# Performance work log

Hardware: AMD Instinct MI355X
Metric: run time of the kernel (lower is better)

## Reference

```python
import jax, jax.numpy as jnp
import numpy as np

# static config (matches init_kwargs)
NH, NKV, E, K = 16, 4, 8, 2
CAP_FACTOR = 1.25
LN_EPS = 1e-5


def _layer_norm(x, w, b):
    mu = jnp.mean(x, axis=-1, keepdims=True)
    var = jnp.mean(jnp.square(x - mu), axis=-1, keepdims=True)
    return (x - mu) * jax.lax.rsqrt(var + LN_EPS) * w + b


def setup_inputs() -> dict:
    key = jax.random.key(0)
    ks = jax.random.split(key, 6)
    S, B, H, F = 2048, 1, 1024, 2048
    HD = H // NH
    qkv_out = NKV * ((NH // NKV) + 2) * HD  # 1536
    f32 = jnp.float32
    return {
        "hidden_states": jax.random.normal(ks[0], (S, B, H), f32),
        "ln1_weight": jnp.ones((H,), f32),
        "ln1_bias": jnp.zeros((H,), f32),
        "ln2_weight": jnp.ones((H,), f32),
        "ln2_bias": jnp.zeros((H,), f32),
        "qkv_weight": jax.random.normal(ks[1], (qkv_out, H), f32) * 0.02,
        "proj_weight": jax.random.normal(ks[2], (H, H), f32) * 0.02,
        "router_weight": jax.random.normal(ks[3], (H, E), f32) * 0.02,
        "moe_w1": jax.random.normal(ks[4], (E, H, F), f32) * 0.02,
        "moe_w2": jax.random.normal(ks[5], (F and E, F, H), f32)[:E] * 0.02 if False else jax.random.normal(ks[5], (E, F, H), f32) * 0.02,
    }


def reference(hidden_states, ln1_weight, ln1_bias, ln2_weight, ln2_bias,
              qkv_weight, proj_weight, router_weight, moe_w1, moe_w2):
    S, B, H = hidden_states.shape
    HD = H // NH
    q_per_kv = NH // NKV
    # ---- attention block (cp_size=1: all-to-alls are identity) ----
    ln1 = _layer_norm(hidden_states, ln1_weight, ln1_bias)
    qkv = jnp.einsum('sbh,oh->sbo', ln1, qkv_weight)
    qkv = qkv.reshape(S, B, NKV, (q_per_kv + 2) * HD)
    q = qkv[..., : q_per_kv * HD].reshape(S, B, NH, HD)
    k = qkv[..., q_per_kv * HD:(q_per_kv + 1) * HD]          # [S,B,NKV,HD]
    v = qkv[..., (q_per_kv + 1) * HD:]                        # [S,B,NKV,HD]
    qb = jnp.transpose(q, (1, 2, 0, 3)).reshape(B, NKV, q_per_kv, S, HD)
    kb = jnp.transpose(k, (1, 2, 0, 3))                       # [B,NKV,S,HD]
    vb = jnp.transpose(v, (1, 2, 0, 3))
    scale = 1.0 / np.sqrt(HD).astype(np.float32)
    scores = jnp.einsum('bgqsd,bgtd->bgqst', qb, kb) * scale  # [B,NKV,qpk,S,S]
    causal = jnp.tril(jnp.ones((S, S), bool))
    scores = jnp.where(causal, scores, jnp.finfo(scores.dtype).min)
    attn = jax.nn.softmax(scores, axis=-1)
    ao = jnp.einsum('bgqst,bgtd->bgqsd', attn, vb)
    ao = ao.reshape(B, NH, S, HD)
    ao = jnp.transpose(ao, (2, 0, 1, 3)).reshape(S, B, H)
    proj = jnp.einsum('sbh,oh->sbo', ao, proj_weight)
    h1 = hidden_states + proj
    # ---- MoE block (ep_size=1: uniform all-to-all is identity) ----
    ln2 = _layer_norm(h1, ln2_weight, ln2_bias)
    x = ln2.reshape(-1, H)                                    # [N,H]
    N = x.shape[0]
    logits = x @ router_weight                                # linear(x, router_weight.t())
    probs = jax.nn.softmax(logits, axis=-1)
    top_p, top_i = jax.lax.top_k(probs, K)
    top_p = top_p / jnp.sum(top_p, axis=-1, keepdims=True)
    exp_idx = top_i.reshape(-1)                               # [N*K]
    exp_p = top_p.reshape(-1)
    # stable sort by expert id, capacity-padded dispatch
    order = jnp.argsort(exp_idx, stable=True)
    sorted_exp = exp_idx[order]
    counts = jnp.bincount(exp_idx, length=E)
    offsets = jnp.concatenate([jnp.zeros((1,), counts.dtype), jnp.cumsum(counts)[:-1]])
    within = jnp.arange(N * K) - offsets[sorted_exp]
    cap = int(np.ceil(N * K / E * CAP_FACTOR))
    T = E * cap
    valid = within < cap
    dst = jnp.where(valid, sorted_exp * cap + within, T)      # T = out-of-bounds -> dropped
    padded_tokens = jnp.zeros((T, H), x.dtype).at[dst].set(x[order // K], mode='drop')
    padded_probs = jnp.zeros((T,), exp_p.dtype).at[dst].set(exp_p[order], mode='drop')
    padded_tid = jnp.zeros((T,), jnp.int32).at[dst].set((order // K).astype(jnp.int32), mode='drop')
    # grouped expert GEMMs: [E,cap,H] x [E,H,F] -> gelu -> [E,cap,H]
    xt = padded_tokens.reshape(E, cap, H)
    fc1 = jax.nn.gelu(jnp.einsum('ech,ehf->ecf', xt, moe_w1))
    fc2 = jnp.einsum('ecf,efh->ech', fc1, moe_w2).reshape(T, H)
    weighted = fc2 * padded_probs[:, None]                    # pad slots have prob 0
    moe_out = jnp.zeros((N, H), hidden_states.dtype).at[padded_tid].add(weighted)
    return h1 + moe_out.reshape(S, B, H)
```

## Files before the change

kernel.cpp:

```cpp
#include <hip/hip_runtime.h>
#include <hip/hip_bf16.h>
#include <stdint.h>

#define S_LEN 2048
#define HDIM  1024
#define NHEAD 16
#define NKVH  4
#define HEADD 64
#define QKV_O 1536
#define NEXP  8
#define TOPK  2
#define CAP   640
#define TCAP  (NEXP*CAP)
#define FDIM  2048
#define LOG2E 1.44269504088896f
#define NCHUNK 40
#define ATTN_BLOCKS (NCHUNK*NHEAD)
#define TRANSP_BLOCKS 4096

typedef __bf16 bf16x8 __attribute__((ext_vector_type(8)));
typedef float  f32x4  __attribute__((ext_vector_type(4)));
typedef unsigned int u32;
typedef u32 u32x4 __attribute__((ext_vector_type(4)));
typedef u32 u32x2 __attribute__((ext_vector_type(2)));
typedef unsigned short u16;
typedef u16 u16x8 __attribute__((ext_vector_type(8)));

__device__ __forceinline__ void gload16(const __bf16* g, __bf16* l) {
    __builtin_amdgcn_global_load_lds(
        (const __attribute__((address_space(1))) u32*)g,
        (__attribute__((address_space(3))) u32*)l, 16, 0, 0);
}

__device__ __constant__ const signed char c_strip[NCHUNK] =
    {0,1,2,3, 4,4, 5,5, 6,6, 7,7, 8,8,8, 9,9,9, 10,10,10, 11,11,11,
     12,12,12,12, 13,13,13,13, 14,14,14,14, 15,15,15,15};
__device__ __constant__ const signed char c_chunk[NCHUNK] =
    {0,0,0,0, 0,1, 0,1, 0,1, 0,1, 0,1,2, 0,1,2, 0,1,2, 0,1,2,
     0,1,2,3, 0,1,2,3, 0,1,2,3, 0,1,2,3};
__device__ __constant__ const signed char c_cbase[16] = {0,1,2,3,4,6,8,10,12,15,18,21,24,28,32,36};
__device__ __constant__ const signed char c_nch[16]   = {1,1,1,1,2,2,2,2,3,3,3,3,4,4,4,4};

__global__ __launch_bounds__(256)
void prep_kernel(const float* __restrict__ hidden, const float* __restrict__ ln1w,
                 const float* __restrict__ ln1bb, const float* __restrict__ qkvW,
                 const float* __restrict__ projW, __bf16* __restrict__ ln1o,
                 __bf16* __restrict__ projWb, __bf16* __restrict__ qkvWb) {
    const int b = blockIdx.x, tid = threadIdx.x;
    if (b < S_LEN) {
        __shared__ float red[256];
        const float* x = hidden + (size_t)b * HDIM;
        float xr[4];
        #pragma unroll
        for (int j = 0; j < 4; ++j) xr[j] = x[tid + 256*j];
        float s = xr[0] + xr[1] + xr[2] + xr[3];
        red[tid] = s; __syncthreads();
        for (int st = 128; st > 0; st >>= 1) { if (tid < st) red[tid] += red[tid+st]; __syncthreads(); }
        float mu = red[0] / HDIM; __syncthreads();
        float v = 0.f;
        #pragma unroll
        for (int j = 0; j < 4; ++j) { float d = xr[j]-mu; v += d*d; }
        red[tid] = v; __syncthreads();
        for (int st = 128; st > 0; st >>= 1) { if (tid < st) red[tid] += red[tid+st]; __syncthreads(); }
        float rstd = rsqrtf(red[0]/HDIM + 1e-5f);
        #pragma unroll
        for (int j = 0; j < 4; ++j) {
            int i = tid + 256*j;
            ln1o[(size_t)b*HDIM + i] = (__bf16)((xr[j]-mu)*rstd*ln1w[i] + ln1bb[i]);
        }
        return;
    }
    const float* src; __bf16* dst; int i;
    if (b < S_LEN + 768) { src = qkvW; dst = qkvWb; i = (b - S_LEN)*256 + tid; }
    else                 { src = projW; dst = projWb; i = (b - S_LEN - 768)*256 + tid; }
    const float4* s = (const float4*)src + (size_t)i*2;
    float4 a = s[0], b4 = s[1];
    __bf16 tmp[8] = {(__bf16)a.x,(__bf16)a.y,(__bf16)a.z,(__bf16)a.w,
                     (__bf16)b4.x,(__bf16)b4.y,(__bf16)b4.z,(__bf16)b4.w};
    *(u32x4*)(dst + (size_t)i*8) = *(u32x4*)tmp;
}

template<int EPI>
__global__ __launch_bounds__(256)
void gemm_bf16_kernel(const __bf16* __restrict__ A, const __bf16* __restrict__ Bt,
                      const float* __restrict__ R, void* __restrict__ Cout,
                      int N, int K, long sA, long sB, long sC) {
    __shared__ __bf16 As[128*64];
    __shared__ __bf16 Bs[128*64];
    const int e = blockIdx.z;
    A  += (size_t)e * sA;
    Bt += (size_t)e * sB;
    const int m0 = blockIdx.y*128, n0 = blockIdx.x*128;
    const int tid = threadIdx.x;
    const int lane = tid & 63, w = tid >> 6;
    const int lr = lane & 15, lg = lane >> 4;
    const int wr = w >> 1, wc = w & 1;
    const int srow8 = lane >> 3, sg = lane & 7;
    f32x4 acc[4][4] = {};
    for (int k0 = 0; k0 < K; k0 += 64) {
        __syncthreads();
        #pragma unroll
        for (int i = 0; i < 4; ++i) {
            int row = 32*w + 8*i + srow8;
            int src_g = sg ^ (row & 7);
            gload16(A  + (size_t)(m0+row)*K + k0 + src_g*8,
                    (__bf16*)((char*)As + (32*w + 8*i)*128));
            gload16(Bt + (size_t)(n0+row)*K + k0 + src_g*8,
                    (__bf16*)((char*)Bs + (32*w + 8*i)*128));
        }
        __syncthreads();
        #pragma unroll
        for (int ks = 0; ks < 2; ++ks) {
            bf16x8 af[4], bfr[4];
            #pragma unroll
            for (int mi = 0; mi < 4; ++mi) {
                int row = wr*64 + mi*16 + lr;
                af[mi] = *(const bf16x8*)((const char*)As + ((row*128 + (lg+4*ks)*16) ^ ((row&7)<<4)));
            }
            #pragma unroll
            for (int ni = 0; ni < 4; ++ni) {
                int row = wc*64 + ni*16 + lr;
                bfr[ni] = *(const bf16x8*)((const char*)Bs + ((row*128 + (lg+4*ks)*16) ^ ((row&7)<<4)));
            }
            #pragma unroll
            for (int mi = 0; mi < 4; ++mi)
                #pragma unroll
                for (int ni = 0; ni < 4; ++ni)
                    acc[mi][ni] = __builtin_amdgcn_mfma_f32_16x16x32_bf16(af[mi], bfr[ni], acc[mi][ni], 0,0,0);
        }
    }
    #pragma unroll
    for (int mi = 0; mi < 4; ++mi) {
        #pragma unroll
        for (int ni = 0; ni < 4; ++ni) {
            #pragma unroll
            for (int r = 0; r < 4; ++r) {
                int row = m0 + wr*64 + mi*16 + lg*4 + r;
                int col = n0 + wc*64 + ni*16 + lr;
                float v = acc[mi][ni][r];
                if (EPI == 1) v += R[(size_t)row*N + col];
                if (EPI == 2) {
                    float t = 0.7978845608028654f * (v + 0.044715f*v*v*v);
                    v = 0.5f * v * (1.f + tanhf(t));
                }
                if (EPI == 2 || EPI == 3)
                    ((__bf16*)Cout)[(size_t)e*sC + (size_t)row*N + col] = (__bf16)v;
                else
                    ((float*)Cout)[(size_t)e*sC + (size_t)row*N + col] = v;
            }
        }
    }
}

template<int EPI>
__global__ __launch_bounds__(256)
void gemm64_bf16_kernel(const __bf16* __restrict__ A, const __bf16* __restrict__ Bt,
                        const float* __restrict__ R, void* __restrict__ Cout,
                        int N, int K, long sA, long sB, long sC) {
    __shared__ __bf16 As[64*64];
    __shared__ __bf16 Bs[128*64];
    const int e = blockIdx.z;
    A  += (size_t)e * sA;
    Bt += (size_t)e * sB;
    const int m0 = blockIdx.y*64, n0 = blockIdx.x*128;
    const int tid = threadIdx.x;
    const int lane = tid & 63, w = tid >> 6;
    const int lr = lane & 15, lg = lane >> 4;
    const int srow8 = lane >> 3, sg = lane & 7;
    f32x4 acc[4][2] = {};
    for (int k0 = 0; k0 < K; k0 += 64) {
        __syncthreads();
        #pragma unroll
        for (int i = 0; i < 2; ++i) {
            int row = 16*w + 8*i + srow8;
            int src_g = sg ^ (row & 7);
            gload16(A + (size_t)(m0+row)*K + k0 + src_g*8,
                    (__bf16*)((char*)As + (16*w + 8*i)*128));
        }
        #pragma unroll
        for (int i = 0; i < 4; ++i) {
            int row = 32*w + 8*i + srow8;
            int src_g = sg ^ (row & 7);
            gload16(Bt + (size_t)(n0+row)*K + k0 + src_g*8,
                    (__bf16*)((char*)Bs + (32*w + 8*i)*128));
        }
        __syncthreads();
        #pragma unroll
        for (int ks = 0; ks < 2; ++ks) {
            bf16x8 af[4], bfr[2];
            #pragma unroll
            for (int mi = 0; mi < 4; ++mi) {
                int row = mi*16 + lr;
                af[mi] = *(const bf16x8*)((const char*)As + ((row*128 + (lg+4*ks)*16) ^ ((row&7)<<4)));
            }
            #pragma unroll
            for (int ni = 0; ni < 2; ++ni) {
                int row = w*32 + ni*16 + lr;
                bfr[ni] = *(const bf16x8*)((const char*)Bs + ((row*128 + (lg+4*ks)*16) ^ ((row&7)<<4)));
            }
            #pragma unroll
            for (int mi = 0; mi < 4; ++mi)
                #pragma unroll
                for (int ni = 0; ni < 2; ++ni)
                    acc[mi][ni] = __builtin_amdgcn_mfma_f32_16x16x32_bf16(af[mi], bfr[ni], acc[mi][ni], 0,0,0);
        }
    }
    #pragma unroll
    for (int mi = 0; mi < 4; ++mi) {
        #pragma unroll
        for (int ni = 0; ni < 2; ++ni) {
            #pragma unroll
            for (int r = 0; r < 4; ++r) {
                int row = m0 + mi*16 + lg*4 + r;
                int col = n0 + w*32 + ni*16 + lr;
                float v = acc[mi][ni][r];
                if (EPI == 1) v += R[(size_t)row*N + col];
                if (EPI == 2) {
                    float t = 0.7978845608028654f * (v + 0.044715f*v*v*v);
                    v = 0.5f * v * (1.f + tanhf(t));
                }
                if (EPI == 2 || EPI == 3)
                    ((__bf16*)Cout)[(size_t)e*sC + (size_t)row*N + col] = (__bf16)v;
                else
                    ((float*)Cout)[(size_t)e*sC + (size_t)row*N + col] = v;
            }
        }
    }
}

__global__ __launch_bounds__(512)
void attn_transp_kernel(const __bf16* __restrict__ qkv, float* __restrict__ partO,
                        float* __restrict__ partML,
                        const float* __restrict__ w1, const float* __restrict__ w2,
                        __bf16* __restrict__ w1t, __bf16* __restrict__ w2t) {
    __shared__ __attribute__((aligned(16))) char smem[49152];
    const int bid = blockIdx.x;
    const bool is_attn = ((bid % 7) == 3) && (bid / 7 < ATTN_BLOCKS);

    if (!is_attn) {
        const int tb = bid - min(ATTN_BLOCKS, (bid + 3) / 7);
        const int half = threadIdx.x >> 8, t256 = threadIdx.x & 255;
        float (*t)[65] = (float(*)[65])(smem + half*16640);
        const int tile = tb*2 + half;
        const float* src; __bf16* dst; int K, N, n0, k0;
        if (tile < 4096) {
            int e = tile >> 9, rem = tile & 511;
            K = HDIM; N = FDIM; n0 = (rem & 31) * 64; k0 = (rem >> 5) * 64;
            src = w1 + (size_t)e*K*N; dst = w1t + (size_t)e*K*N;
        } else {
            int tt = tile - 4096; int e = tt >> 9, rem = tt & 511;
            K = FDIM; N = HDIM; n0 = (rem & 15) * 64; k0 = (rem >> 4) * 64;
            src = w2 + (size_t)e*K*N; dst = w2t + (size_t)e*K*N;
        }
        const int r = t256 >> 4, c4 = (t256 & 15) * 4;
        #pragma unroll
        for (int i = 0; i < 4; ++i) {
            float4 v = *(const float4*)(src + (size_t)(k0 + r + 16*i)*N + n0 + c4);
            t[r+16*i][c4+0] = v.x; t[r+16*i][c4+1] = v.y;
            t[r+16*i][c4+2] = v.z; t[r+16*i][c4+3] = v.w;
        }
        __syncthreads();
        const int rn = t256 >> 3, kc = (t256 & 7) * 8;
        #pragma unroll
        for (int i = 0; i < 2; ++i) {
            int n = rn + 32*i;
            __bf16 tmp[8];
            #pragma unroll
            for (int j = 0; j < 8; ++j) tmp[j] = (__bf16)t[kc+j][n];
            *(u32x4*)(dst + (size_t)(n0+n)*K + k0 + kc) = *(u32x4*)tmp;
        }
        return;
    }

    __bf16* Kls = (__bf16*)smem;
    __bf16* Vls = (__bf16*)(smem + 16384);
    const int a = bid / 7;
    const int cx = a % NCHUNK;
    const int h  = a / NCHUNK;
    const int hg = h >> 2, qi = h & 3;
    const int qb = c_strip[cx];
    const int t0 = 4 * c_chunk[cx];
    const int t1 = min(qb + 1, t0 + 4);
    const int q0 = qb * 128;
    const int tid  = threadIdx.x;
    const int w    = tid >> 6;
    const int lane = tid & 63;
    const int lr   = lane & 15;
    const int lg   = lane >> 4;

    const int krow = tid >> 2, kc = (tid & 3) * 2;
    const int va = tid & 63,  dg  = tid >> 6;
    u32x4 kreg[2]; u16x8 vreg[2];

    const __bf16* kbase = qkv + hg*384 + 256;
    const __bf16* vbase = qkv + hg*384 + 320;

#define ISSUE(T) do { \
        const __bf16* kp = kbase + (size_t)((T)*128 + krow)*QKV_O + kc*8; \
        kreg[0] = *(const u32x4*)(kp); \
        kreg[1] = *(const u32x4*)(kp + 8); \
        const __bf16* vp = vbase + (size_t)((T)*128 + 2*va)*QKV_O + dg*8; \
        vreg[0] = *(const u16x8*)(vp); \
        vreg[1] = *(const u16x8*)(vp + QKV_O); \
    } while(0)

#define COMMIT() do { \
        char* Kb = (char*)Kls; \
        *(u32x4*)(Kb + ((krow*128 + (kc+0)*16) ^ ((krow&7)<<4))) = kreg[0]; \
        *(u32x4*)(Kb + ((krow*128 + (kc+1)*16) ^ ((krow&7)<<4))) = kreg[1]; \
        char* Vb = (char*)Vls; \
        _Pragma("unroll") \
        for (int j = 0; j < 8; ++j) { \
            int d = dg*8 + j; \
            u32 u = ((u32)vreg[1][j] << 16) | vreg[0][j]; \
            *(u32*)(Vb + ((d*256 + va*4) ^ ((d&7)<<4))) = u; \
        } \
    } while(0)

    const int qrow = q0 + w*16 + lr;
    const __bf16* qp = qkv + (size_t)qrow*QKV_O + hg*384 + qi*64;
    bf16x8 qfrag[2];
    #pragma unroll
    for (int ks = 0; ks < 2; ++ks) {
        bf16x8 qr = *(const bf16x8*)(qp + ks*32 + lg*8);
        #pragma unroll
        for (int j = 0; j < 8; ++j) qfrag[ks][j] = (__bf16)((float)qr[j] * 0.125f);
    }
    bf16x8 ones;
    #pragma unroll
    for (int j = 0; j < 8; ++j) ones[j] = (__bf16)1.0f;

    f32x4 oacc[4] = {};
    f32x4 lcol = {};
    float mrow[4] = {-INFINITY,-INFINITY,-INFINITY,-INFINITY};

    ISSUE(t0);
    for (int t = t0; t < t1; ++t) {
        __syncthreads();
        COMMIT();
        if (t+1 < t1) ISSUE(t+1);
        __syncthreads();

        f32x4 sacc[8] = {};
        const char* Kb = (const char*)Kls;
        #pragma unroll
        for (int f = 0; f < 8; ++f) {
            int row = lr + 16*f;
            int swz = (row & 7) << 4;
            #pragma unroll
            for (int ks = 0; ks < 2; ++ks) {
                bf16x8 kf = *(const bf16x8*)(Kb + ((row*128 + (lg*8+32*ks)*2) ^ swz));
                sacc[f] = __builtin_amdgcn_mfma_f32_16x16x32_bf16(qfrag[ks], kf, sacc[f], 0,0,0);
            }
        }
        if (t == qb) {
            #pragma unroll
            for (int f = 0; f < 8; ++f)
                #pragma unroll
                for (int r = 0; r < 4; ++r)
                    if (lr + 16*f > 16*w + 4*lg + r) sacc[f][r] = -INFINITY;
        }
        float tm[4];
        #pragma unroll
        for (int r = 0; r < 4; ++r) {
            float a2 = fmaxf(fmaxf(sacc[0][r], sacc[1][r]), fmaxf(sacc[2][r], sacc[3][r]));
            float b2 = fmaxf(fmaxf(sacc[4][r], sacc[5][r]), fmaxf(sacc[6][r], sacc[7][r]));
            tm[r] = fmaxf(a2, b2);
        }
        #pragma unroll
        for (int msk = 1; msk < 16; msk <<= 1)
            #pragma unroll
            for (int r = 0; r < 4; ++r) tm[r] = fmaxf(tm[r], __shfl_xor(tm[r], msk, 64));
        float corr[4];
        #pragma unroll
        for (int r = 0; r < 4; ++r) {
            float mn = fmaxf(mrow[r], tm[r]);
            corr[r] = exp2f((mrow[r]-mn)*LOG2E);
            mrow[r] = mn;
        }
        #pragma unroll
        for (int f = 0; f < 8; ++f)
            #pragma unroll
            for (int r = 0; r < 4; ++r)
                sacc[f][r] = exp2f((sacc[f][r]-mrow[r])*LOG2E);
        #pragma unroll
        for (int ct = 0; ct < 4; ++ct)
            #pragma unroll
            for (int r = 0; r < 4; ++r) oacc[ct][r] *= corr[r];
        #pragma unroll
        for (int r = 0; r < 4; ++r) lcol[r] *= corr[r];

        char* Pw = smem + 32768 + w*2048;
        const char* Vb = (const char*)Vls;
        #pragma unroll
        for (int half = 0; half < 2; ++half) {
            #pragma unroll
            for (int f = 0; f < 4; ++f)
                #pragma unroll
                for (int r = 0; r < 4; ++r) {
                    int row = 4*lg + r, col = lr + 16*f;
                    *(__bf16*)(Pw + ((row*128 + col*2) ^ ((row&7)<<4))) = (__bf16)sacc[4*half+f][r];
                }
            bf16x8 pa[2];
            #pragma unroll
            for (int ks = 0; ks < 2; ++ks)
                pa[ks] = *(const bf16x8*)(Pw + ((lr*128 + (lg*8+32*ks)*2) ^ ((lr&7)<<4)));
            #pragma unroll
            for (int ks = 0; ks < 2; ++ks)
                lcol = __builtin_amdgcn_mfma_f32_16x16x32_bf16(pa[ks], ones, lcol, 0,0,0);
            #pragma unroll
            for (int ct = 0; ct < 4; ++ct) {
                int row = lr + 16*ct;
                int swz = (row & 7) << 4;
                #pragma unroll
                for (int ks = 0; ks < 2; ++ks) {
                    int gks = 2*half + ks;
                    bf16x8 vf = *(const bf16x8*)(Vb + ((row*256 + (lg*8+32*gks)*2) ^ swz));
                    oacc[ct] = __builtin_amdgcn_mfma_f32_16x16x32_bf16(pa[ks], vf, oacc[ct], 0,0,0);
                }
            }
        }
    }
    const int p = h*NCHUNK + cx;
    float* po = partO + (size_t)p * (128*64);
    #pragma unroll
    for (int ct = 0; ct < 4; ++ct)
        #pragma unroll
        for (int r = 0; r < 4; ++r)
            po[(16*w + 4*lg + r)*64 + 16*ct + lr] = oacc[ct][r];
    if (lr == 0) {
        float* pm = partML + (size_t)p * 256;
        #pragma unroll
        for (int r = 0; r < 4; ++r) {
            pm[(16*w + 4*lg + r)*2    ] = mrow[r];
            pm[(16*w + 4*lg + r)*2 + 1] = lcol[r];
        }
    }
#undef ISSUE
#undef COMMIT
}

__global__ __launch_bounds__(256)
void attn_combine_kernel(const float* __restrict__ partO, const float* __restrict__ partML,
                         __bf16* __restrict__ ao) {
    const int rb = blockIdx.x, h = blockIdx.y;
    const int row0 = rb*8;
    const int qb = row0 >> 7;
    const int nc = c_nch[qb], cb = c_cbase[qb];
    const int tid = threadIdx.x;
    const int rl = tid >> 5, d2 = (tid & 31) * 2;
    const int grow = row0 + rl;
    const int srow = grow & 127;
    const int pbase = h*NCHUNK + cb;
    float mv[4], lv[4];
    float M = -INFINITY;
    for (int c = 0; c < nc; ++c) {
        const float* pm = partML + (size_t)(pbase+c)*256 + srow*2;
        mv[c] = pm[0]; lv[c] = pm[1];
        M = fmaxf(M, mv[c]);
    }
    float L = 0.f, a0 = 0.f, a1 = 0.f;
    for (int c = 0; c < nc; ++c) {
        float wc = exp2f((mv[c]-M)*LOG2E);
        L += wc * lv[c];
        const float* po = partO + (size_t)(pbase+c)*(128*64) + srow*64 + d2;
        a0 += wc * po[0];
        a1 += wc * po[1];
    }
    float inv = 1.f / L;
    __bf16 o2[2] = {(__bf16)(a0*inv), (__bf16)(a1*inv)};
    *(u32*)(ao + (size_t)grow*HDIM + h*64 + d2) = *(u32*)o2;
}

__global__ __launch_bounds__(256)
void ln2_router_kernel(const float* __restrict__ h1, const float* __restrict__ w,
                       const float* __restrict__ b, const float* __restrict__ rw,
                       __bf16* __restrict__ x2b, int* __restrict__ expi,
                       float* __restrict__ expp) {
    const int t = blockIdx.x, tid = threadIdx.x;
    __shared__ float red[256];
    __shared__ float red8[256][8];
    const float* x = h1 + (size_t)t*HDIM;
    float xr[4];
    #pragma unroll
    for (int j = 0; j < 4; ++j) xr[j] = x[tid + 256*j];
    float s = xr[0] + xr[1] + xr[2] + xr[3];
    red[tid] = s; __syncthreads();
    for (int st = 128; st > 0; st >>= 1) { if (tid < st) red[tid] += red[tid+st]; __syncthreads(); }
    float mu = red[0] / HDIM; __syncthreads();
    float v = 0.f;
    #pragma unroll
    for (int j = 0; j < 4; ++j) { float d = xr[j]-mu; v += d*d; }
    red[tid] = v; __syncthreads();
    for (int st = 128; st > 0; st >>= 1) { if (tid < st) red[tid] += red[tid+st]; __syncthreads(); }
    float rstd = rsqrtf(red[0]/HDIM + 1e-5f);
    float part[8] = {};
    #pragma unroll
    for (int j = 0; j < 4; ++j) {
        int i = tid + 256*j;
        float o = (xr[j]-mu)*rstd*w[i] + b[i];
        x2b[(size_t)t*HDIM + i] = (__bf16)o;
        const float* wp = rw + (size_t)i*NEXP;
        #pragma unroll
        for (int e2 = 0; e2 < 8; ++e2) part[e2] += o * wp[e2];
    }
    #pragma unroll
    for (int e2 = 0; e2 < 8; ++e2) red8[tid][e2] = part[e2];
    __syncthreads();
    for (int st = 128; st > 0; st >>= 1) {
        if (tid < st)
            #pragma unroll
            for (int e2 = 0; e2 < 8; ++e2) red8[tid][e2] += red8[tid+st][e2];
        __syncthreads();
    }
    if (tid == 0) {
        float lg[8];
        #pragma unroll
        for (int e2 = 0; e2 < 8; ++e2) lg[e2] = red8[0][e2];
        int i0 = 0;
        for (int e2 = 1; e2 < 8; ++e2) if (lg[e2] > lg[i0]) i0 = e2;
        int i1 = -1;
        for (int e2 = 0; e2 < 8; ++e2) { if (e2 == i0) continue; if (i1 < 0 || lg[e2] > lg[i1]) i1 = e2; }
        float p1 = __expf(lg[i1] - lg[i0]);
        float inv = 1.f / (1.f + p1);
        expi[t*2]   = i0; expi[t*2+1] = i1;
        expp[t*2]   = inv; expp[t*2+1] = p1 * inv;
    }
}

__global__ __launch_bounds__(256)
void dst_fast_kernel(const int* __restrict__ expi, int* __restrict__ dst) {
    __shared__ int hist[256][9];
    const int tid = threadIdx.x;
    int ev[16];
    #pragma unroll
    for (int i = 0; i < 16; i += 4)
        *(int4*)(ev+i) = *(const int4*)(expi + tid*16 + i);
    int cnt[8] = {};
    #pragma unroll
    for (int i = 0; i < 16; ++i)
        #pragma unroll
        for (int e = 0; e < 8; ++e) cnt[e] += (ev[i] == e);
    #pragma unroll
    for (int e = 0; e < 8; ++e) hist[tid][e] = cnt[e];
    __syncthreads();
    const int w = tid >> 6, lane = tid & 63;
    #pragma unroll
    for (int rep = 0; rep < 2; ++rep) {
        int e = w + rep*4;
        int h0 = hist[4*lane+0][e], h1 = hist[4*lane+1][e],
            h2 = hist[4*lane+2][e], h3 = hist[4*lane+3][e];
        int s = h0+h1+h2+h3, inc = s;
        #pragma unroll
        for (int off = 1; off < 64; off <<= 1) {
            int v = __shfl_up(inc, off, 64);
            if (lane >= off) inc += v;
        }
        int excl = inc - s;
        hist[4*lane+0][e] = excl;
        hist[4*lane+1][e] = excl + h0;
        hist[4*lane+2][e] = excl + h0 + h1;
        hist[4*lane+3][e] = excl + h0 + h1 + h2;
    }
    __syncthreads();
    int run[8];
    #pragma unroll
    for (int e = 0; e < 8; ++e) run[e] = hist[tid][e];
    int out[16];
    #pragma unroll
    for (int i = 0; i < 16; ++i) {
        int e = ev[i], within = 0;
        #pragma unroll
        for (int e2 = 0; e2 < 8; ++e2)
            if (e == e2) { within = run[e2]; run[e2]++; }
        out[i] = (within < CAP) ? (e*CAP + within) : -1;
    }
    #pragma unroll
    for (int i = 0; i < 16; i += 4)
        *(int4*)(dst + tid*16 + i) = *(const int4*)(out+i);
}

__global__ void scatter_kernel(const __bf16* __restrict__ x2b, const int* __restrict__ dst,
                               __bf16* __restrict__ xt) {
    int s = blockIdx.x;
    int d = dst[s];
    if (d < 0) return;
    int t = s >> 1;
    int i = threadIdx.x;
    u32x2 v = *(const u32x2*)(x2b + (size_t)t*HDIM + i*4);
    *(u32x2*)(xt + (size_t)d*HDIM + i*4) = v;
}

__global__ void combine_kernel(const float* __restrict__ h1, const float* __restrict__ fc2,
                               const int* __restrict__ dst, const float* __restrict__ expp,
                               float* __restrict__ out) {
    int t = blockIdx.x;
    int d0 = dst[t*2], d1 = dst[t*2+1];
    float p0 = expp[t*2], p1 = expp[t*2+1];
    int i = threadIdx.x * 4;
    float4 v = *(const float4*)(h1 + (size_t)t*HDIM + i);
    if (d0 >= 0) {
        float4 f = *(const float4*)(fc2 + (size_t)d0*HDIM + i);
        v.x += p0*f.x; v.y += p0*f.y; v.z += p0*f.z; v.w += p0*f.w;
    }
    if (d1 >= 0) {
        float4 f = *(const float4*)(fc2 + (size_t)d1*HDIM + i);
        v.x += p1*f.x; v.y += p1*f.y; v.z += p1*f.z; v.w += p1*f.w;
    }
    *(float4*)(out + (size_t)t*HDIM + i) = v;
}

extern "C" void kernel_launch(void* const* d_in, const int* in_sizes, int n_in,
                              void* d_out, int out_size, void* d_ws, size_t ws_size,
                              hipStream_t stream) {
    const float* hidden = (const float*)d_in[0];
    const float* ln1w   = (const float*)d_in[1];
    const float* ln1b_  = (const float*)d_in[2];
    const float* ln2w   = (const float*)d_in[3];
    const float* ln2b_  = (const float*)d_in[4];
    const float* qkvW   = (const float*)d_in[5];
    const float* projW  = (const float*)d_in[6];
    const float* routW  = (const float*)d_in[7];
    const float* w1     = (const float*)d_in[8];
    const float* w2     = (const float*)d_in[9];
    float* out = (float*)d_out;

    char* base = (char*)d_ws;
    __bf16* w1t    = (__bf16*)(base);
    __bf16* w2t    = (__bf16*)(base + 33554432);
    __bf16* ln1b   = (__bf16*)(base);
    __bf16* qkvWb  = (__bf16*)(base + 4194304);
    char* B0 = base + 67108864;
    float*  h1   = (float*)(B0);
    __bf16* xtb  = (__bf16*)(B0 + 8388608);
    __bf16* fc1b = (__bf16*)(B0 + 18874368);
    float*  fc2  = (float*)(B0 + 39845888);
    __bf16* x2b    = (__bf16*)fc2;
    __bf16* qkvb   = (__bf16*)((char*)fc2 + 4194304);
    __bf16* aob    = (__bf16*)((char*)fc2 + 10485760);
    __bf16* projWb = (__bf16*)((char*)fc2 + 14680064);
    int*    expi = (int*)(B0 + 60817408);
    int*    dsts = (int*)(B0 + 60833792);
    float*  expp = (float*)(B0 + 60850176);
    float*  partML = (float*)xtb;
    float*  partO  = (float*)fc1b;

    prep_kernel<<<S_LEN + 768 + 512, 256, 0, stream>>>(
        hidden, ln1w, ln1b_, qkvW, projW, ln1b, projWb, qkvWb);
    gemm64_bf16_kernel<3><<<dim3(QKV_O/128, S_LEN/64, 1), 256, 0, stream>>>(
        ln1b, qkvWb, nullptr, qkvb, QKV_O, HDIM, 0, 0, 0);
    attn_transp_kernel<<<ATTN_BLOCKS + TRANSP_BLOCKS, 512, 0, stream>>>(
        qkvb, partO, partML, w1, w2, w1t, w2t);
    attn_combine_kernel<<<dim3(S_LEN/8, NHEAD), 256, 0, stream>>>(partO, partML, aob);
    gemm64_bf16_kernel<1><<<dim3(HDIM/128, S_LEN/64, 1), 256, 0, stream>>>(
        aob, projWb, hidden, h1, HDIM, HDIM, 0, 0, 0);
    ln2_router_kernel<<<S_LEN, 256, 0, stream>>>(h1, ln2w, ln2b_, routW, x2b, expi, expp);
    dst_fast_kernel<<<1, 256, 0, stream>>>(expi, dsts);
    scatter_kernel<<<S_LEN*TOPK, 256, 0, stream>>>(x2b, dsts, xtb);
    gemm_bf16_kernel<2><<<dim3(FDIM/128, CAP/128, NEXP), 256, 0, stream>>>(
        xtb, w1t, nullptr, fc1b, FDIM, HDIM,
        (long)CAP*HDIM, (long)FDIM*HDIM, (long)CAP*FDIM);
    gemm64_bf16_kernel<0><<<dim3(HDIM/128, CAP/64, NEXP), 256, 0, stream>>>(
        fc1b, w2t, nullptr, fc2, HDIM, FDIM,
        (long)CAP*FDIM, (long)FDIM*HDIM, (long)CAP*HDIM);
    combine_kernel<<<S_LEN, 256, 0, stream>>>(h1, fc2, dsts, expp, out);
}
```

Before: 229.3 us.

## Drop MoE weight transpose; read row-major bf16 weights in new GEMM kernel

The fp32 expert weights are now converted to bf16 in their original [K,N] layout instead of being transposed through shared memory. A new GEMM variant loads the B operand with plain register loads one tile ahead, then interleaves pairs of K rows into the swizzled LDS layout itself. Both MoE GEMMs use it, and the FC1 GEMM moves from 128-row to 64-row M tiles. This removes the costly LDS transpose pass from the attention/conversion kernel. In exchange the expert GEMMs do more scalar LDS writes and lose the async global-to-LDS load for B.

Measured after the change: 295.2 us. +28.7%, slower.

```diff
diff --git a/kernel.cpp b/kernel.cpp
--- a/kernel.cpp
+++ b/kernel.cpp
@@ -16,7 +16,7 @@
 #define LOG2E 1.44269504088896f
 #define NCHUNK 40
 #define ATTN_BLOCKS (NCHUNK*NHEAD)
-#define TRANSP_BLOCKS 4096
+#define CONV_BLOCKS 8192
 
 typedef __bf16 bf16x8 __attribute__((ext_vector_type(8)));
 typedef float  f32x4  __attribute__((ext_vector_type(4)));
@@ -78,78 +78,6 @@
     __bf16 tmp[8] = {(__bf16)a.x,(__bf16)a.y,(__bf16)a.z,(__bf16)a.w,
                      (__bf16)b4.x,(__bf16)b4.y,(__bf16)b4.z,(__bf16)b4.w};
     *(u32x4*)(dst + (size_t)i*8) = *(u32x4*)tmp;
-}
-
-template<int EPI>
-__global__ __launch_bounds__(256)
-void gemm_bf16_kernel(const __bf16* __restrict__ A, const __bf16* __restrict__ Bt,
-                      const float* __restrict__ R, void* __restrict__ Cout,
-                      int N, int K, long sA, long sB, long sC) {
-    __shared__ __bf16 As[128*64];
-    __shared__ __bf16 Bs[128*64];
-    const int e = blockIdx.z;
-    A  += (size_t)e * sA;
-    Bt += (size_t)e * sB;
-    const int m0 = blockIdx.y*128, n0 = blockIdx.x*128;
-    const int tid = threadIdx.x;
-    const int lane = tid & 63, w = tid >> 6;
-    const int lr = lane & 15, lg = lane >> 4;
-    const int wr = w >> 1, wc = w & 1;
-    const int srow8 = lane >> 3, sg = lane & 7;
-    f32x4 acc[4][4] = {};
-    for (int k0 = 0; k0 < K; k0 += 64) {
-        __syncthreads();
-        #pragma unroll
-        for (int i = 0; i < 4; ++i) {
-            int row = 32*w + 8*i + srow8;
-            int src_g = sg ^ (row & 7);
-            gload16(A  + (size_t)(m0+row)*K + k0 + src_g*8,
-                    (__bf16*)((char*)As + (32*w + 8*i)*128));
-            gload16(Bt + (size_t)(n0+row)*K + k0 + src_g*8,
-                    (__bf16*)((char*)Bs + (32*w + 8*i)*128));
-        }
-        __syncthreads();
-        #pragma unroll
-        for (int ks = 0; ks < 2; ++ks) {
-            bf16x8 af[4], bfr[4];
-            #pragma unroll
-            for (int mi = 0; mi < 4; ++mi) {
-                int row = wr*64 + mi*16 + lr;
-                af[mi] = *(const bf16x8*)((const char*)As + ((row*128 + (lg+4*ks)*16) ^ ((row&7)<<4)));
-            }
-            #pragma unroll
-            for (int ni = 0; ni < 4; ++ni) {
-                int row = wc*64 + ni*16 + lr;
-                bfr[ni] = *(const bf16x8*)((const char*)Bs + ((row*128 + (lg+4*ks)*16) ^ ((row&7)<<4)));
-            }
-            #pragma unroll
-            for (int mi = 0; mi < 4; ++mi)
-                #pragma unroll
-                for (int ni = 0; ni < 4; ++ni)
-                    acc[mi][ni] = __builtin_amdgcn_mfma_f32_16x16x32_bf16(af[mi], bfr[ni], acc[mi][ni], 0,0,0);
-        }
-    }
-    #pragma unroll
-    for (int mi = 0; mi < 4; ++mi) {
-        #pragma unroll
-        for (int ni = 0; ni < 4; ++ni) {
-            #pragma unroll
-            for (int r = 0; r < 4; ++r) {
-                int row = m0 + wr*64 + mi*16 + lg*4 + r;
-                int col = n0 + wc*64 + ni*16 + lr;
-                float v = acc[mi][ni][r];
-                if (EPI == 1) v += R[(size_t)row*N + col];
-                if (EPI == 2) {
-                    float t = 0.7978845608028654f * (v + 0.044715f*v*v*v);
-                    v = 0.5f * v * (1.f + tanhf(t));
-                }
-                if (EPI == 2 || EPI == 3)
-                    ((__bf16*)Cout)[(size_t)e*sC + (size_t)row*N + col] = (__bf16)v;
-                else
-                    ((float*)Cout)[(size_t)e*sC + (size_t)row*N + col] = v;
-            }
-        }
-    }
 }
 
 template<int EPI>
@@ -228,53 +156,133 @@
     }
 }
 
+template<int EPI>
+__global__ __launch_bounds__(256)
+void gemm64t_bf16_kernel(const __bf16* __restrict__ A, const __bf16* __restrict__ Wb,
+                         const float* __restrict__ R, void* __restrict__ Cout,
+                         int N, int K, long sA, long sB, long sC) {
+    __shared__ __bf16 As[64*64];
+    __shared__ __bf16 Bs[128*64];
+    const int e = blockIdx.z;
+    A  += (size_t)e * sA;
+    Wb += (size_t)e * sB;
+    const int m0 = blockIdx.y*64, n0 = blockIdx.x*128;
+    const int tid = threadIdx.x;
+    const int lane = tid & 63, w = tid >> 6;
+    const int lr = lane & 15, lg = lane >> 4;
+    const int srow8 = lane >> 3, sg = lane & 7;
+    const int nc = tid & 7, kp = tid >> 3;
+    u16x8 wr0a, wr0b, wr1a, wr1b;
+
+#define ISSUE_B(K0) do { \
+        const __bf16* p = Wb + (size_t)((K0) + 2*kp)*N + n0 + nc*16; \
+        wr0a = *(const u16x8*)(p); \
+        wr0b = *(const u16x8*)(p + 8); \
+        wr1a = *(const u16x8*)(p + N); \
+        wr1b = *(const u16x8*)(p + N + 8); \
+    } while(0)
+
+#define COMMIT_B() do { \
+        _Pragma("unroll") \
+        for (int j = 0; j < 8; ++j) { \
+            int n = nc*16 + j; \
+            u32 u = ((u32)wr1a[j] << 16) | wr0a[j]; \
+            *(u32*)((char*)Bs + ((n*128 + kp*4) ^ ((n&7)<<4))) = u; \
+        } \
+        _Pragma("unroll") \
+        for (int j = 0; j < 8; ++j) { \
+            int n = nc*16 + 8 + j; \
+            u32 u = ((u32)wr1b[j] << 16) | wr0b[j]; \
+            *(u32*)((char*)Bs + ((n*128 + kp*4) ^ ((n&7)<<4))) = u; \
+        } \
+    } while(0)
+
+    f32x4 acc[4][2] = {};
+    ISSUE_B(0);
+    for (int k0 = 0; k0 < K; k0 += 64) {
+        __syncthreads();
+        COMMIT_B();
+        #pragma unroll
+        for (int i = 0; i < 2; ++i) {
+            int row = 16*w + 8*i + srow8;
+            int src_g = sg ^ (row & 7);
+            gload16(A + (size_t)(m0+row)*K + k0 + src_g*8,
+                    (__bf16*)((char*)As + (16*w + 8*i)*128));
+        }
+        if (k0 + 64 < K) ISSUE_B(k0 + 64);
+        __syncthreads();
+        #pragma unroll
+        for (int ks = 0; ks < 2; ++ks) {
+            bf16x8 af[4], bfr[2];
+            #pragma unroll
+            for (int mi = 0; mi < 4; ++mi) {
+                int row = mi*16 + lr;
+                af[mi] = *(const bf16x8*)((const char*)As + ((row*128 + (lg+4*ks)*16) ^ ((row&7)<<4)));
+            }
+            #pragma unroll
+            for (int ni = 0; ni < 2; ++ni) {
+                int row = w*32 + ni*16 + lr;
+                bfr[ni] = *(const bf16x8*)((const char*)Bs + ((row*128 + (lg+4*ks)*16) ^ ((row&7)<<4)));
+            }
+            #pragma unroll
+            for (int mi = 0; mi < 4; ++mi)
+                #pragma unroll
+                for (int ni = 0; ni < 2; ++ni)
+                    acc[mi][ni] = __builtin_amdgcn_mfma_f32_16x16x32_bf16(af[mi], bfr[ni], acc[mi][ni], 0,0,0);
+        }
+    }
+#undef ISSUE_B
+#undef COMMIT_B
+    #pragma unroll
+    for (int mi = 0; mi < 4; ++mi) {
+        #pragma unroll
+        for (int ni = 0; ni < 2; ++ni) {
+            #pragma unroll
+            for (int r = 0; r < 4; ++r) {
+                int row = m0 + mi*16 + lg*4 + r;
+                int col = n0 + w*32 + ni*16 + lr;
+                float v = acc[mi][ni][r];
+                if (EPI == 1) v += R[(size_t)row*N + col];
+                if (EPI == 2) {
+                    float t = 0.7978845608028654f * (v + 0.044715f*v*v*v);
+                    v = 0.5f * v * (1.f + tanhf(t));
+                }
+                if (EPI == 2 || EPI == 3)
+                    ((__bf16*)Cout)[(size_t)e*sC + (size_t)row*N + col] = (__bf16)v;
+                else
+                    ((float*)Cout)[(size_t)e*sC + (size_t)row*N + col] = v;
+            }
+        }
+    }
+}
+
 __global__ __launch_bounds__(512)
-void attn_transp_kernel(const __bf16* __restrict__ qkv, float* __restrict__ partO,
-                        float* __restrict__ partML,
-                        const float* __restrict__ w1, const float* __restrict__ w2,
-                        __bf16* __restrict__ w1t, __bf16* __restrict__ w2t) {
+void attn_conv_kernel(const __bf16* __restrict__ qkv, float* __restrict__ partO,
+                      float* __restrict__ partML,
+                      const float* __restrict__ w1, const float* __restrict__ w2,
+                      __bf16* __restrict__ w1b, __bf16* __restrict__ w2b) {
     __shared__ __attribute__((aligned(16))) char smem[49152];
     const int bid = blockIdx.x;
-    const bool is_attn = ((bid % 7) == 3) && (bid / 7 < ATTN_BLOCKS);
+    const bool is_attn = ((bid % 13) == 6) && (bid / 13 < ATTN_BLOCKS);
 
     if (!is_attn) {
-        const int tb = bid - min(ATTN_BLOCKS, (bid + 3) / 7);
-        const int half = threadIdx.x >> 8, t256 = threadIdx.x & 255;
-        float (*t)[65] = (float(*)[65])(smem + half*16640);
-        const int tile = tb*2 + half;
-        const float* src; __bf16* dst; int K, N, n0, k0;
-        if (tile < 4096) {
-            int e = tile >> 9, rem = tile & 511;
-            K = HDIM; N = FDIM; n0 = (rem & 31) * 64; k0 = (rem >> 5) * 64;
-            src = w1 + (size_t)e*K*N; dst = w1t + (size_t)e*K*N;
-        } else {
-            int tt = tile - 4096; int e = tt >> 9, rem = tt & 511;
-            K = FDIM; N = HDIM; n0 = (rem & 15) * 64; k0 = (rem >> 4) * 64;
-            src = w2 + (size_t)e*K*N; dst = w2t + (size_t)e*K*N;
-        }
-        const int r = t256 >> 4, c4 = (t256 & 15) * 4;
-        #pragma unroll
-        for (int i = 0; i < 4; ++i) {
-            float4 v = *(const float4*)(src + (size_t)(k0 + r + 16*i)*N + n0 + c4);
-            t[r+16*i][c4+0] = v.x; t[r+16*i][c4+1] = v.y;
-            t[r+16*i][c4+2] = v.z; t[r+16*i][c4+3] = v.w;
-        }
-        __syncthreads();
-        const int rn = t256 >> 3, kc = (t256 & 7) * 8;
-        #pragma unroll
-        for (int i = 0; i < 2; ++i) {
-            int n = rn + 32*i;
-            __bf16 tmp[8];
-            #pragma unroll
-            for (int j = 0; j < 8; ++j) tmp[j] = (__bf16)t[kc+j][n];
-            *(u32x4*)(dst + (size_t)(n0+n)*K + k0 + kc) = *(u32x4*)tmp;
-        }
+        const int cv = bid - min(ATTN_BLOCKS, (bid + 6) / 13);
+        const float* src; __bf16* dst;
+        size_t off;
+        if (cv < 4096) { src = w1; dst = w1b; off = (size_t)cv * 4096; }
+        else           { src = w2; dst = w2b; off = (size_t)(cv - 4096) * 4096; }
+        const int i = threadIdx.x;
+        const float4* s = (const float4*)(src + off) + (size_t)i*2;
+        float4 a = s[0], b4 = s[1];
+        __bf16 tmp[8] = {(__bf16)a.x,(__bf16)a.y,(__bf16)a.z,(__bf16)a.w,
+                         (__bf16)b4.x,(__bf16)b4.y,(__bf16)b4.z,(__bf16)b4.w};
+        *(u32x4*)(dst + off + (size_t)i*8) = *(u32x4*)tmp;
         return;
     }
 
     __bf16* Kls = (__bf16*)smem;
     __bf16* Vls = (__bf16*)(smem + 16384);
-    const int a = bid / 7;
+    const int a = bid / 13;
     const int cx = a % NCHUNK;
     const int h  = a / NCHUNK;
     const int hg = h >> 2, qi = h & 3;
@@ -626,8 +634,8 @@
     float* out = (float*)d_out;
 
     char* base = (char*)d_ws;
-    __bf16* w1t    = (__bf16*)(base);
-    __bf16* w2t    = (__bf16*)(base + 33554432);
+    __bf16* w1b    = (__bf16*)(base);
+    __bf16* w2b    = (__bf16*)(base + 33554432);
     __bf16* ln1b   = (__bf16*)(base);
     __bf16* qkvWb  = (__bf16*)(base + 4194304);
     char* B0 = base + 67108864;
@@ -649,19 +657,19 @@
         hidden, ln1w, ln1b_, qkvW, projW, ln1b, projWb, qkvWb);
     gemm64_bf16_kernel<3><<<dim3(QKV_O/128, S_LEN/64, 1), 256, 0, stream>>>(
         ln1b, qkvWb, nullptr, qkvb, QKV_O, HDIM, 0, 0, 0);
-    attn_transp_kernel<<<ATTN_BLOCKS + TRANSP_BLOCKS, 512, 0, stream>>>(
-        qkvb, partO, partML, w1, w2, w1t, w2t);
+    attn_conv_kernel<<<ATTN_BLOCKS + CONV_BLOCKS, 512, 0, stream>>>(
+        qkvb, partO, partML, w1, w2, w1b, w2b);
     attn_combine_kernel<<<dim3(S_LEN/8, NHEAD), 256, 0, stream>>>(partO, partML, aob);
     gemm64_bf16_kernel<1><<<dim3(HDIM/128, S_LEN/64, 1), 256, 0, stream>>>(
         aob, projWb, hidden, h1, HDIM, HDIM, 0, 0, 0);
     ln2_router_kernel<<<S_LEN, 256, 0, stream>>>(h1, ln2w, ln2b_, routW, x2b, expi, expp);
     dst_fast_kernel<<<1, 256, 0, stream>>>(expi, dsts);
     scatter_kernel<<<S_LEN*TOPK, 256, 0, stream>>>(x2b, dsts, xtb);
-    gemm_bf16_kernel<2><<<dim3(FDIM/128, CAP/128, NEXP), 256, 0, stream>>>(
-        xtb, w1t, nullptr, fc1b, FDIM, HDIM,
-        (long)CAP*HDIM, (long)FDIM*HDIM, (long)CAP*FDIM);
-    gemm64_bf16_kernel<0><<<dim3(HDIM/128, CAP/64, NEXP), 256, 0, stream>>>(
-        fc1b, w2t, nullptr, fc2, HDIM, FDIM,
+    gemm64t_bf16_kernel<2><<<dim3(FDIM/128, CAP/64, NEXP), 256, 0, stream>>>(
+        xtb, w1b, nullptr, fc1b, FDIM, HDIM,
+        (long)CAP*HDIM, (long)HDIM*FDIM, (long)CAP*FDIM);
+    gemm64t_bf16_kernel<0><<<dim3(HDIM/128, CAP/64, NEXP), 256, 0, stream>>>(
+        fc1b, w2b, nullptr, fc2, HDIM, FDIM,
         (long)CAP*FDIM, (long)FDIM*HDIM, (long)CAP*HDIM);
     combine_kernel<<<S_LEN, 256, 0, stream>>>(h1, fc2, dsts, expp, out);
 }
```

## Move part of w2 weight transpose into projection GEMM kernel

Applied to the files above, without the earlier changes.

The fused attention/transpose kernel now handles only 3072 transpose blocks (6144 tiles). The remaining 2048 w2 tiles move into a new proj_transp_kernel, which runs the projection GEMM with residual on its first 256 blocks and the transpose on the rest. The attention block interleaving changes from every 7th to every 5th block to match the smaller grid. The aim is to balance the transpose work so it overlaps with the under-filled projection GEMM instead of lengthening the attention phase.

Result: faster. 222.0 us (-3.2%).

```diff
diff --git a/kernel.cpp b/kernel.cpp
--- a/kernel.cpp
+++ b/kernel.cpp
@@ -16,7 +16,7 @@
 #define LOG2E 1.44269504088896f
 #define NCHUNK 40
 #define ATTN_BLOCKS (NCHUNK*NHEAD)
-#define TRANSP_BLOCKS 4096
+#define FUSED_TRANSP 3072
 
 typedef __bf16 bf16x8 __attribute__((ext_vector_type(8)));
 typedef float  f32x4  __attribute__((ext_vector_type(4)));
@@ -228,6 +228,99 @@
     }
 }
 
+__global__ __launch_bounds__(256)
+void proj_transp_kernel(const __bf16* __restrict__ A, const __bf16* __restrict__ Bt,
+                        const float* __restrict__ R, float* __restrict__ Cout,
+                        const float* __restrict__ w2, __bf16* __restrict__ w2t) {
+    __shared__ __attribute__((aligned(16))) char smem[24576];
+    const int bid = blockIdx.x, tid = threadIdx.x;
+    if (bid >= 256) {
+        float (*t)[65] = (float(*)[65])smem;
+        const int tile = 6144 + (bid - 256);
+        const int tt = tile - 4096;
+        const int e = tt >> 9, rem = tt & 511;
+        const int K = FDIM, N = HDIM;
+        const int n0 = (rem & 15) * 64, k0 = (rem >> 4) * 64;
+        const float* src = w2 + (size_t)e*K*N;
+        __bf16* dst = w2t + (size_t)e*K*N;
+        const int r = tid >> 4, c4 = (tid & 15) * 4;
+        #pragma unroll
+        for (int i = 0; i < 4; ++i) {
+            float4 v = *(const float4*)(src + (size_t)(k0 + r + 16*i)*N + n0 + c4);
+            t[r+16*i][c4+0] = v.x; t[r+16*i][c4+1] = v.y;
+            t[r+16*i][c4+2] = v.z; t[r+16*i][c4+3] = v.w;
+        }
+        __syncthreads();
+        const int rn = tid >> 3, kc = (tid & 7) * 8;
+        #pragma unroll
+        for (int i = 0; i < 2; ++i) {
+            int n = rn + 32*i;
+            __bf16 tmp[8];
+            #pragma unroll
+            for (int j = 0; j < 8; ++j) tmp[j] = (__bf16)t[kc+j][n];
+            *(u32x4*)(dst + (size_t)(n0+n)*K + k0 + kc) = *(u32x4*)tmp;
+        }
+        return;
+    }
+    __bf16* As = (__bf16*)smem;
+    __bf16* Bs = (__bf16*)(smem + 8192);
+    const int N = HDIM, K = HDIM;
+    const int m0 = (bid >> 3)*64, n0 = (bid & 7)*128;
+    const int lane = tid & 63, w = tid >> 6;
+    const int lr = lane & 15, lg = lane >> 4;
+    const int srow8 = lane >> 3, sg = lane & 7;
+    f32x4 acc[4][2] = {};
+    for (int k0 = 0; k0 < K; k0 += 64) {
+        __syncthreads();
+        #pragma unroll
+        for (int i = 0; i < 2; ++i) {
+            int row = 16*w + 8*i + srow8;
+            int src_g = sg ^ (row & 7);
+            gload16(A + (size_t)(m0+row)*K + k0 + src_g*8,
+                    (__bf16*)((char*)As + (16*w + 8*i)*128));
+        }
+        #pragma unroll
+        for (int i = 0; i < 4; ++i) {
+            int row = 32*w + 8*i + srow8;
+            int src_g = sg ^ (row & 7);
+            gload16(Bt + (size_t)(n0+row)*K + k0 + src_g*8,
+                    (__bf16*)((char*)Bs + (32*w + 8*i)*128));
+        }
+        __syncthreads();
+        #pragma unroll
+        for (int ks = 0; ks < 2; ++ks) {
+            bf16x8 af[4], bfr[2];
+            #pragma unroll
+            for (int mi = 0; mi < 4; ++mi) {
+                int row = mi*16 + lr;
+                af[mi] = *(const bf16x8*)((const char*)As + ((row*128 + (lg+4*ks)*16) ^ ((row&7)<<4)));
+            }
+            #pragma unroll
+            for (int ni = 0; ni < 2; ++ni) {
+                int row = w*32 + ni*16 + lr;
+                bfr[ni] = *(const bf16x8*)((const char*)Bs + ((row*128 + (lg+4*ks)*16) ^ ((row&7)<<4)));
+            }
+            #pragma unroll
+            for (int mi = 0; mi < 4; ++mi)
+                #pragma unroll
+                for (int ni = 0; ni < 2; ++ni)
+                    acc[mi][ni] = __builtin_amdgcn_mfma_f32_16x16x32_bf16(af[mi], bfr[ni], acc[mi][ni], 0,0,0);
+        }
+    }
+    #pragma unroll
+    for (int mi = 0; mi < 4; ++mi) {
+        #pragma unroll
+        for (int ni = 0; ni < 2; ++ni) {
+            #pragma unroll
+            for (int r = 0; r < 4; ++r) {
+                int row = m0 + mi*16 + lg*4 + r;
+                int col = n0 + w*32 + ni*16 + lr;
+                Cout[(size_t)row*N + col] = acc[mi][ni][r] + R[(size_t)row*N + col];
+            }
+        }
+    }
+}
+
 __global__ __launch_bounds__(512)
 void attn_transp_kernel(const __bf16* __restrict__ qkv, float* __restrict__ partO,
                         float* __restrict__ partML,
@@ -235,10 +328,10 @@
                         __bf16* __restrict__ w1t, __bf16* __restrict__ w2t) {
     __shared__ __attribute__((aligned(16))) char smem[49152];
     const int bid = blockIdx.x;
-    const bool is_attn = ((bid % 7) == 3) && (bid / 7 < ATTN_BLOCKS);
+    const bool is_attn = ((bid % 5) == 3) && (bid / 5 < ATTN_BLOCKS);
 
     if (!is_attn) {
-        const int tb = bid - min(ATTN_BLOCKS, (bid + 3) / 7);
+        const int tb = bid - min(ATTN_BLOCKS, (bid + 2) / 5);
         const int half = threadIdx.x >> 8, t256 = threadIdx.x & 255;
         float (*t)[65] = (float(*)[65])(smem + half*16640);
         const int tile = tb*2 + half;
@@ -274,7 +367,7 @@
 
     __bf16* Kls = (__bf16*)smem;
     __bf16* Vls = (__bf16*)(smem + 16384);
-    const int a = bid / 7;
+    const int a = bid / 5;
     const int cx = a % NCHUNK;
     const int h  = a / NCHUNK;
     const int hg = h >> 2, qi = h & 3;
@@ -649,11 +742,11 @@
         hidden, ln1w, ln1b_, qkvW, projW, ln1b, projWb, qkvWb);
     gemm64_bf16_kernel<3><<<dim3(QKV_O/128, S_LEN/64, 1), 256, 0, stream>>>(
         ln1b, qkvWb, nullptr, qkvb, QKV_O, HDIM, 0, 0, 0);
-    attn_transp_kernel<<<ATTN_BLOCKS + TRANSP_BLOCKS, 512, 0, stream>>>(
+    attn_transp_kernel<<<ATTN_BLOCKS + FUSED_TRANSP, 512, 0, stream>>>(
         qkvb, partO, partML, w1, w2, w1t, w2t);
     attn_combine_kernel<<<dim3(S_LEN/8, NHEAD), 256, 0, stream>>>(partO, partML, aob);
-    gemm64_bf16_kernel<1><<<dim3(HDIM/128, S_LEN/64, 1), 256, 0, stream>>>(
-        aob, projWb, hidden, h1, HDIM, HDIM, 0, 0, 0);
+    proj_transp_kernel<<<256 + 2048, 256, 0, stream>>>(
+        aob, projWb, hidden, h1, w2, w2t);
     ln2_router_kernel<<<S_LEN, 256, 0, stream>>>(h1, ln2w, ln2b_, routW, x2b, expi, expp);
     dst_fast_kernel<<<1, 256, 0, stream>>>(expi, dsts);
     scatter_kernel<<<S_LEN*TOPK, 256, 0, stream>>>(x2b, dsts, xtb);
```
